# Optimization experiments

Measured on AMD Instinct MI355X. Metric: run time of the kernel, lower is better.

The kernel has to match this reference:

```python
import jax, jax.numpy as jnp
import numpy as np

B, D, C, N = 256, 512, 345, 50000
K = 5
ALPHA = 1.0
EPS = 1e-12


def setup_inputs() -> dict:
    key = jax.random.key(0)
    k1, k2, k3, k4, k5 = jax.random.split(key, 5)
    return {
        "features": jax.random.normal(k1, (B, D), dtype=jnp.float32),
        "predictions": jax.random.normal(k2, (B, C), dtype=jnp.float32),
        "fea_bank": jax.random.normal(k3, (N, D), dtype=jnp.float32),
        "score_bank": jax.random.uniform(k4, (N, C), dtype=jnp.float32, minval=1e-3, maxval=1.0),
        "trg_idx": jax.random.randint(k5, (B,), 0, N, dtype=jnp.int64),
    }


def reference(features, predictions, fea_bank, score_bank, trg_idx):
    softmax_out = jax.nn.softmax(predictions, axis=1)  # [B, C]

    # --- no_grad block: bank update + neighbor retrieval ---
    f_norm = features / jnp.maximum(
        jnp.linalg.norm(features, axis=1, keepdims=True), EPS
    )
    f_ng = jax.lax.stop_gradient(f_norm)
    s_ng = jax.lax.stop_gradient(softmax_out)
    fb = fea_bank.at[trg_idx].set(f_ng)       # [N, D]
    sb = score_bank.at[trg_idx].set(s_ng)     # [N, C]
    distance = f_ng @ fb.T                    # [B, N] cosine similarity
    _, idx_near = jax.lax.top_k(distance, K + 1)
    idx_near = idx_near[:, 1:]                # drop self -> [B, K]
    score_near = sb[idx_near]                 # [B, K, C]

    # F.kl_div(input=softmax_out (NOT log), target=score_near):
    # target * (log(target) - input), summed over C and K, mean over B.
    kl = score_near * (jnp.log(score_near) - softmax_out[:, None, :])
    loss = jnp.mean(kl.sum(-1).sum(-1))

    # dispersion: masked pairwise dot of softmax outputs (off-diagonal)
    dot = softmax_out @ softmax_out.T         # [B, B]
    mask = 1.0 - jnp.eye(B, dtype=dot.dtype)
    neg_pred = jnp.mean((dot * mask).sum(-1))
    loss = loss + ALPHA * neg_pred
    return loss
```

## Files before the change

kernel.cpp:

```cpp
#include <hip/hip_runtime.h>
#include <cstdint>

#define BB 256
#define DD 512
#define CC 345
#define NBANK 50000
#define NPAD 50048
#define KNEI 5
#define ALPHAC 1.0f
#define EPSN 1e-12f
#define NTILES 391

typedef short short8 __attribute__((ext_vector_type(8)));
typedef float f32x4 __attribute__((ext_vector_type(4)));

__device__ inline uint32_t f2bf1(float x) {
    union { float f; uint32_t u; } v; v.f = x;
    return (v.u + 0x7FFFu + ((v.u >> 16) & 1u)) >> 16;
}
__device__ inline uint32_t pack2(float a, float b) {
    return f2bf1(a) | (f2bf1(b) << 16);
}
__device__ inline float bl(uint32_t x) {
    union { uint32_t u; float f; } v; v.u = x << 16; return v.f;
}
__device__ inline float bh(uint32_t x) {
    union { uint32_t u; float f; } v; v.u = x & 0xFFFF0000u; return v.f;
}
__device__ inline bool better(float v1, int i1, float v2, int i2) {
    return (v1 > v2) || (v1 == v2 && i1 < i2);
}
__device__ inline void ins6(float v, int j, float* lv, int* li) {
    if (better(v, j, lv[5], li[5])) {
        int q = 5;
        while (q > 0 && better(v, j, lv[q - 1], li[q - 1])) {
            lv[q] = lv[q - 1]; li[q] = li[q - 1]; q--;
        }
        lv[q] = v; li[q] = j;
    }
}
__device__ inline void tree6(float* sv, int* si, int t, const float* lv, const int* li) {
#pragma unroll
    for (int r = 0; r < 6; r++) { sv[t * 6 + r] = lv[r]; si[t * 6 + r] = li[r]; }
    __syncthreads();
    for (int s = 128; s > 0; s >>= 1) {
        if (t < s) {
            float av[6], bv[6], rv[6];
            int ai[6], bi[6], ri[6];
#pragma unroll
            for (int r = 0; r < 6; r++) {
                av[r] = sv[t * 6 + r];       ai[r] = si[t * 6 + r];
                bv[r] = sv[(t + s) * 6 + r]; bi[r] = si[(t + s) * 6 + r];
            }
            int x = 0, y = 0;
#pragma unroll
            for (int o = 0; o < 6; o++) {
                if (better(av[x], ai[x], bv[y], bi[y])) { rv[o] = av[x]; ri[o] = ai[x]; x++; }
                else                                    { rv[o] = bv[y]; ri[o] = bi[y]; y++; }
            }
#pragma unroll
            for (int r = 0; r < 6; r++) { sv[t * 6 + r] = rv[r]; si[t * 6 + r] = ri[r]; }
        }
        __syncthreads();
    }
}
__device__ inline void async16(const void* g, void* l) {
    __builtin_amdgcn_global_load_lds(
        (const __attribute__((address_space(1))) unsigned int*)g,
        (__attribute__((address_space(3))) unsigned int*)l, 16, 0, 0);
}
__device__ inline size_t sw_off(int tile, int r, int ch) {
    return (size_t)tile * 8192 + r * 64 + ((ch ^ (r & 7)) * 8);
}

__global__ void winner_kernel(const int* __restrict__ trg, int* __restrict__ win,
                              float* __restrict__ out) {
    int t = threadIdx.x;
    if (t == 0) out[0] = 0.f;
    int mv = trg[t];
    int w = 1;
    for (int b2 = t + 1; b2 < BB; b2++)
        if (trg[b2] == mv) w = 0;
    win[t] = w;
}

__global__ void norm_softmax_kernel(const float* __restrict__ feat,
                                    const float* __restrict__ pred,
                                    unsigned short* __restrict__ fnb,
                                    unsigned short* __restrict__ fnb2,
                                    float* __restrict__ p) {
    int b = blockIdx.x, t = threadIdx.x;
    __shared__ float red[256];
    float x0 = feat[b * DD + t];
    float x1 = feat[b * DD + t + 256];
    red[t] = x0 * x0 + x1 * x1;
    __syncthreads();
    for (int s = 128; s > 0; s >>= 1) {
        if (t < s) red[t] += red[t + s];
        __syncthreads();
    }
    float inv = 1.0f / fmaxf(sqrtf(red[0]), EPSN);
    if (t < 64) {
        const f32x4* src = (const f32x4*)(feat + b * DD + t * 8);
        f32x4 f0 = src[0], f1 = src[1];
        uint4 u = make_uint4(pack2(f0[0] * inv, f0[1] * inv),
                             pack2(f0[2] * inv, f0[3] * inv),
                             pack2(f1[0] * inv, f1[1] * inv),
                             pack2(f1[2] * inv, f1[3] * inv));
        *(uint4*)(fnb + b * DD + t * 8) = u;
        int mtile = b >> 7, r = b & 127, kt = t >> 3, ch = t & 7;
        *(uint4*)(fnb2 + sw_off(mtile * 8 + kt, r, ch)) = u;
    }
    __syncthreads();
    float y0 = (t < CC) ? pred[b * CC + t] : -3.0e38f;
    float y1 = (t + 256 < CC) ? pred[b * CC + t + 256] : -3.0e38f;
    red[t] = fmaxf(y0, y1);
    __syncthreads();
    for (int s = 128; s > 0; s >>= 1) {
        if (t < s) red[t] = fmaxf(red[t], red[t + s]);
        __syncthreads();
    }
    float M = red[0];
    __syncthreads();
    float e0 = (t < CC) ? expf(y0 - M) : 0.f;
    float e1 = (t + 256 < CC) ? expf(y1 - M) : 0.f;
    red[t] = e0 + e1;
    __syncthreads();
    for (int s = 128; s > 0; s >>= 1) {
        if (t < s) red[t] += red[t + s];
        __syncthreads();
    }
    float si = 1.0f / red[0];
    if (t < CC) p[b * CC + t] = e0 * si;
    if (t + 256 < CC) p[b * CC + t + 256] = e1 * si;
}

__global__ void convert_kernel(const float* __restrict__ bank,
                               unsigned short* __restrict__ bankb) {
    int tid = blockIdx.x * 256 + threadIdx.x;
    int j = tid >> 6, c = tid & 63;
    int kt = c >> 3, ch = c & 7;
    int r = j & 127, nt = j >> 7;
    uint4 val = make_uint4(0, 0, 0, 0);
    if (j < NBANK) {
        const f32x4* s = (const f32x4*)(bank + (size_t)j * DD + kt * 64 + ch * 8);
        f32x4 f0 = s[0], f1 = s[1];
        val = make_uint4(pack2(f0[0], f0[1]), pack2(f0[2], f0[3]),
                         pack2(f1[0], f1[1]), pack2(f1[2], f1[3]));
    }
    *(uint4*)(bankb + sw_off(nt * 8 + kt, r, ch)) = val;
}

__global__ void patch_kernel(const unsigned short* __restrict__ fnb,
                             const int* __restrict__ trg, const int* __restrict__ win,
                             unsigned short* __restrict__ bankb) {
    int b = blockIdx.x;
    if (!win[b]) return;
    int t = threadIdx.x;
    int j = trg[b];
    int nt = j >> 7, r = j & 127, kt = t >> 3, ch = t & 7;
    uint4 v = *(const uint4*)(fnb + b * DD + t * 8);
    *(uint4*)(bankb + sw_off(nt * 8 + kt, r, ch)) = v;
}

__global__ __launch_bounds__(256) void gemm_topk_kernel(
        const unsigned short* __restrict__ fnb2, const unsigned short* __restrict__ bankb,
        float* __restrict__ tilemax) {
    __shared__ __align__(16) char smem[32768];
    unsigned short* As = (unsigned short*)smem;
    unsigned short* Bs = (unsigned short*)(smem + 16384);

    int t = threadIdx.x;
    int ntb = blockIdx.x >> 1, mtile = blockIdx.x & 1;
    int w = t >> 6, lane = t & 63, quad = lane >> 4, l16 = lane & 15;
    int wm = w >> 1, wn = w & 1;
    int j0 = ntb * 128;

    f32x4 acc[4][4];
#pragma unroll
    for (int mt = 0; mt < 4; mt++)
#pragma unroll
        for (int nt = 0; nt < 4; nt++)
            acc[mt][nt] = (f32x4){0.f, 0.f, 0.f, 0.f};

    const char* Ag = (const char*)fnb2 + (size_t)mtile * 8 * 16384;
    const char* Bg = (const char*)bankb + (size_t)ntb * 8 * 16384;

    for (int kt = 0; kt < 8; kt++) {
        size_t tb = (size_t)kt * 16384;
        int co = w * 4096 + lane * 16;
#pragma unroll
        for (int u = 0; u < 4; u++)
            async16(Ag + tb + co + u * 1024, smem + w * 4096 + u * 1024);
#pragma unroll
        for (int u = 0; u < 4; u++)
            async16(Bg + tb + co + u * 1024, smem + 16384 + w * 4096 + u * 1024);
        __syncthreads();
#pragma unroll
        for (int ks = 0; ks < 2; ks++) {
            int sw = ((ks * 4 + quad) ^ (l16 & 7)) * 8;
            short8 af[4], bf[4];
#pragma unroll
            for (int mt = 0; mt < 4; mt++)
                af[mt] = *(const short8*)(As + (wm * 64 + mt * 16 + l16) * 64 + sw);
#pragma unroll
            for (int nt = 0; nt < 4; nt++)
                bf[nt] = *(const short8*)(Bs + (wn * 64 + nt * 16 + l16) * 64 + sw);
#pragma unroll
            for (int mt = 0; mt < 4; mt++)
#pragma unroll
                for (int nt = 0; nt < 4; nt++)
                    acc[mt][nt] = __builtin_amdgcn_mfma_f32_16x16x32_bf16(
                        af[mt], bf[nt], acc[mt][nt], 0, 0, 0);
        }
        __syncthreads();
    }

    bool maskPad[4] = {false, false, false, false};
    if (ntb == NTILES - 1) {
#pragma unroll
        for (int nt = 0; nt < 4; nt++)
            maskPad[nt] = (j0 + wn * 64 + nt * 16 + l16) >= NBANK;
    }
    float* sm = (float*)smem;
#pragma unroll
    for (int mt = 0; mt < 4; mt++)
#pragma unroll
        for (int r2 = 0; r2 < 4; r2++) {
            float m = -3.4e38f;
#pragma unroll
            for (int nt = 0; nt < 4; nt++) {
                float v = maskPad[nt] ? -3.4e38f : acc[mt][nt][r2];
                m = fmaxf(m, v);
            }
#pragma unroll
            for (int off = 1; off < 16; off <<= 1)
                m = fmaxf(m, __shfl_xor(m, off, 64));
            if (l16 == 0) sm[(wm * 64 + mt * 16 + quad * 4 + r2) * 2 + wn] = m;
        }
    __syncthreads();
    if (t < 128)
        tilemax[(size_t)ntb * 256 + mtile * 128 + t] = fmaxf(sm[t * 2], sm[t * 2 + 1]);
}

__global__ void merge_rescan_kernel(const unsigned short* __restrict__ fnb,
                                    const unsigned short* __restrict__ bankb,
                                    const float* __restrict__ tilemax,
                                    int* __restrict__ nidx) {
    int i = blockIdx.x, t = threadIdx.x;
    __shared__ float a[512];
    __shared__ float tm[512];
    __shared__ int cand[NTILES + 1];
    __shared__ int ncand;
    __shared__ float sv[1536];
    __shared__ int si[1536];

    uint32_t wrd = ((const uint32_t*)(fnb + (size_t)i * DD))[t];
    a[2 * t] = bl(wrd);
    a[2 * t + 1] = bh(wrd);
    tm[t] = (t < NTILES) ? tilemax[(size_t)t * 256 + i] : -3.4e38f;
    tm[t + 256] = (t + 256 < NTILES) ? tilemax[(size_t)(t + 256) * 256 + i] : -3.4e38f;
    if (t == 0) ncand = 0;
    __syncthreads();

    float lv[6]; int li[6];
#pragma unroll
    for (int r = 0; r < 6; r++) { lv[r] = -3.4e38f; li[r] = 0x7FFFFFFF; }
    ins6(tm[t], t, lv, li);
    ins6(tm[t + 256], t + 256, lv, li);
    tree6(sv, si, t, lv, li);
    float M6 = sv[5];
    __syncthreads();

    if (t < NTILES && tm[t] >= M6) cand[atomicAdd(&ncand, 1)] = t;
    if (t + 256 < NTILES && tm[t + 256] >= M6) cand[atomicAdd(&ncand, 1)] = t + 256;
    __syncthreads();
    int nc = ncand;

#pragma unroll
    for (int r = 0; r < 6; r++) { lv[r] = -3.4e38f; li[r] = 0x7FFFFFFF; }
    int r = t & 127;
    int rx = r & 7;
    for (int c0 = 0; c0 < nc; c0 += 2) {
        int slot = c0 + (t >> 7);
        if (slot < nc) {
            int nt = cand[slot];
            int j = nt * 128 + r;
            if (j < NBANK) {
                float dot = 0.f;
#pragma unroll
                for (int kt = 0; kt < 8; kt++) {
                    const uint4* q = (const uint4*)(bankb + (size_t)(nt * 8 + kt) * 8192 + r * 64);
                    const float* ab = a + kt * 64;
#pragma unroll
                    for (int pp = 0; pp < 8; pp++) {
                        uint4 u = q[pp];
                        const float* av = ab + ((pp ^ rx) << 3);
                        dot += bl(u.x) * av[0] + bh(u.x) * av[1]
                             + bl(u.y) * av[2] + bh(u.y) * av[3]
                             + bl(u.z) * av[4] + bh(u.z) * av[5]
                             + bl(u.w) * av[6] + bh(u.w) * av[7];
                    }
                }
                ins6(dot, j, lv, li);
            }
        }
    }
    tree6(sv, si, t, lv, li);
    if (t == 0) {
#pragma unroll
        for (int rr = 1; rr < 6; rr++) nidx[i * KNEI + rr - 1] = si[rr];
    }
}

__global__ void kl_negpred_kernel(const float* __restrict__ p,
                                  const float* __restrict__ sbank,
                                  const int* __restrict__ nidx,
                                  const int* __restrict__ trg,
                                  float* __restrict__ out) {
    int bid = blockIdx.x, t = threadIdx.x;
    __shared__ float red[256];
    __shared__ float aux[256];
    if (bid < BB) {
        int b = bid;
        __shared__ int sj[KNEI], sb[KNEI];
        if (t < KNEI) {
            int j = nidx[b * KNEI + t];
            sj[t] = j;
            int src = -1;
            for (int b2 = 0; b2 < BB; b2++)
                if (trg[b2] == j) src = b2;
            sb[t] = src;
        }
        __syncthreads();
        float local = 0.f;
        for (int k = 0; k < KNEI; k++) {
            int j = sj[k], src = sb[k];
            const float* srow = (src >= 0) ? (p + src * CC) : (sbank + (size_t)j * CC);
            for (int c = t; c < CC; c += 256) {
                float s = srow[c];
                local += s * (logf(s) - p[b * CC + c]);
            }
        }
        red[t] = local;
        __syncthreads();
        for (int s = 128; s > 0; s >>= 1) {
            if (t < s) red[t] += red[t + s];
            __syncthreads();
        }
        if (t == 0) atomicAdd(out, red[0] * (1.0f / BB));
    } else {
        int c = bid - BB;
        float v = p[t * CC + c];
        red[t] = v;
        aux[t] = v * v;
        __syncthreads();
        for (int s = 128; s > 0; s >>= 1) {
            if (t < s) { red[t] += red[t + s]; aux[t] += aux[t + s]; }
            __syncthreads();
        }
        if (t == 0) atomicAdd(out, ALPHAC * (red[0] * red[0] - aux[0]) * (1.0f / BB));
    }
}

extern "C" void kernel_launch(void* const* d_in, const int* in_sizes, int n_in,
                              void* d_out, int out_size, void* d_ws, size_t ws_size,
                              hipStream_t stream) {
    const float* feat  = (const float*)d_in[0];
    const float* pred  = (const float*)d_in[1];
    const float* bank  = (const float*)d_in[2];
    const float* sbank = (const float*)d_in[3];
    const int*   trg   = (const int*)d_in[4];
    float* out = (float*)d_out;

    char* ws = (char*)d_ws;
    unsigned short* fnb2    = (unsigned short*)ws;
    unsigned short* fnb     = (unsigned short*)(ws + 262144);
    unsigned short* bankb   = (unsigned short*)(ws + 524288);
    float*          p       = (float*)(ws + 51773440);
    int*            win     = (int*)(ws + 52126720);
    float*          tilemax = (float*)(ws + 52127744);
    int*            nidx    = (int*)(ws + 52528128);

    winner_kernel<<<1, 256, 0, stream>>>(trg, win, out);
    norm_softmax_kernel<<<BB, 256, 0, stream>>>(feat, pred, fnb, fnb2, p);
    convert_kernel<<<(NPAD * 64) / 256, 256, 0, stream>>>(bank, bankb);
    patch_kernel<<<BB, 64, 0, stream>>>(fnb, trg, win, bankb);
    gemm_topk_kernel<<<NTILES * 2, 256, 0, stream>>>(fnb2, bankb, tilemax);
    merge_rescan_kernel<<<BB, 256, 0, stream>>>(fnb, bankb, tilemax, nidx);
    kl_negpred_kernel<<<BB + CC, 256, 0, stream>>>(p, sbank, nidx, trg, out);
}
```

Baseline: 292.0 us.

## Emit per-half-tile top-2 keys from GEMM to shrink rescan in merge

The GEMM epilogue now records, for each row and each 64-column half tile, the top two packed (value, index) 64-bit keys instead of a single tile max. The merge kernel selects the top 6 among these keys and rescans only the half tiles whose second-best key reaches the sixth-best threshold, which should usually be none. The goal is to remove most of the exact dot-product rescan over whole 128-column candidate tiles. It also stages trg in shared memory in two small kernels. In exchange it writes a larger candidate buffer and caps the rescan list at 128 half tiles.

After: 284.3 us. 2.6% less time.

```diff
diff --git a/kernel.cpp b/kernel.cpp
--- a/kernel.cpp
+++ b/kernel.cpp
@@ -10,9 +10,12 @@
 #define ALPHAC 1.0f
 #define EPSN 1e-12f
 #define NTILES 391
+#define NHALF (NTILES * 2)
+#define CSLOTS (NTILES * 4)
 
 typedef short short8 __attribute__((ext_vector_type(8)));
 typedef float f32x4 __attribute__((ext_vector_type(4)));
+typedef unsigned long long u64;
 
 __device__ inline uint32_t f2bf1(float x) {
     union { float f; uint32_t u; } v; v.f = x;
@@ -27,39 +30,43 @@
 __device__ inline float bh(uint32_t x) {
     union { uint32_t u; float f; } v; v.u = x & 0xFFFF0000u; return v.f;
 }
-__device__ inline bool better(float v1, int i1, float v2, int i2) {
-    return (v1 > v2) || (v1 == v2 && i1 < i2);
-}
-__device__ inline void ins6(float v, int j, float* lv, int* li) {
-    if (better(v, j, lv[5], li[5])) {
+__device__ inline u64 mkkey(float v, int j) {
+    union { float f; uint32_t u; } c; c.f = v;
+    uint32_t b = c.u;
+    uint32_t k = (b & 0x80000000u) ? ~b : (b | 0x80000000u);
+    return ((u64)k << 32) | (uint32_t)(~j);
+}
+__device__ inline u64 umax64(u64 a, u64 b) { return a > b ? a : b; }
+__device__ inline u64 shfl_xor_u64(u64 v, int m) {
+    int lo = __shfl_xor((int)(uint32_t)v, m, 64);
+    int hi = __shfl_xor((int)(v >> 32), m, 64);
+    return ((u64)(uint32_t)hi << 32) | (uint32_t)lo;
+}
+__device__ inline void ins6u(u64 k, u64* lv) {
+    if (k > lv[5]) {
         int q = 5;
-        while (q > 0 && better(v, j, lv[q - 1], li[q - 1])) {
-            lv[q] = lv[q - 1]; li[q] = li[q - 1]; q--;
-        }
-        lv[q] = v; li[q] = j;
-    }
-}
-__device__ inline void tree6(float* sv, int* si, int t, const float* lv, const int* li) {
-#pragma unroll
-    for (int r = 0; r < 6; r++) { sv[t * 6 + r] = lv[r]; si[t * 6 + r] = li[r]; }
+        while (q > 0 && k > lv[q - 1]) { lv[q] = lv[q - 1]; q--; }
+        lv[q] = k;
+    }
+}
+__device__ inline void tree6u(u64* sv, int t, const u64* lv) {
+#pragma unroll
+    for (int r = 0; r < 6; r++) sv[t * 6 + r] = lv[r];
     __syncthreads();
     for (int s = 128; s > 0; s >>= 1) {
         if (t < s) {
-            float av[6], bv[6], rv[6];
-            int ai[6], bi[6], ri[6];
-#pragma unroll
-            for (int r = 0; r < 6; r++) {
-                av[r] = sv[t * 6 + r];       ai[r] = si[t * 6 + r];
-                bv[r] = sv[(t + s) * 6 + r]; bi[r] = si[(t + s) * 6 + r];
+            u64 av[6], bv[6], rv[6];
+#pragma unroll
+            for (int r = 0; r < 6; r++) { av[r] = sv[t * 6 + r]; bv[r] = sv[(t + s) * 6 + r]; }
+            int x = 0, y = 0;
+#pragma unroll
+            for (int o = 0; o < 6; o++) {
+                bool pk = av[x] > bv[y];
+                rv[o] = pk ? av[x] : bv[y];
+                x += pk; y += !pk;
             }
-            int x = 0, y = 0;
-#pragma unroll
-            for (int o = 0; o < 6; o++) {
-                if (better(av[x], ai[x], bv[y], bi[y])) { rv[o] = av[x]; ri[o] = ai[x]; x++; }
-                else                                    { rv[o] = bv[y]; ri[o] = bi[y]; y++; }
-            }
-#pragma unroll
-            for (int r = 0; r < 6; r++) { sv[t * 6 + r] = rv[r]; si[t * 6 + r] = ri[r]; }
+#pragma unroll
+            for (int r = 0; r < 6; r++) sv[t * 6 + r] = rv[r];
         }
         __syncthreads();
     }
@@ -76,11 +83,14 @@
 __global__ void winner_kernel(const int* __restrict__ trg, int* __restrict__ win,
                               float* __restrict__ out) {
     int t = threadIdx.x;
+    __shared__ int st[BB];
     if (t == 0) out[0] = 0.f;
-    int mv = trg[t];
+    st[t] = trg[t];
+    __syncthreads();
+    int mv = st[t];
     int w = 1;
     for (int b2 = t + 1; b2 < BB; b2++)
-        if (trg[b2] == mv) w = 0;
+        if (st[b2] == mv) w = 0;
     win[t] = w;
 }
 
@@ -165,7 +175,7 @@
 
 __global__ __launch_bounds__(256) void gemm_topk_kernel(
         const unsigned short* __restrict__ fnb2, const unsigned short* __restrict__ bankb,
-        float* __restrict__ tilemax) {
+        u64* __restrict__ cand) {
     __shared__ __align__(16) char smem[32768];
     unsigned short* As = (unsigned short*)smem;
     unsigned short* Bs = (unsigned short*)(smem + 16384);
@@ -216,100 +226,110 @@
         __syncthreads();
     }
 
-    bool maskPad[4] = {false, false, false, false};
-    if (ntb == NTILES - 1) {
-#pragma unroll
-        for (int nt = 0; nt < 4; nt++)
-            maskPad[nt] = (j0 + wn * 64 + nt * 16 + l16) >= NBANK;
-    }
-    float* sm = (float*)smem;
+    bool maskPad[4];
+#pragma unroll
+    for (int nt = 0; nt < 4; nt++)
+        maskPad[nt] = (ntb == NTILES - 1) && ((j0 + wn * 64 + nt * 16 + l16) >= NBANK);
+
 #pragma unroll
     for (int mt = 0; mt < 4; mt++)
 #pragma unroll
         for (int r2 = 0; r2 < 4; r2++) {
-            float m = -3.4e38f;
+            u64 k[4];
 #pragma unroll
             for (int nt = 0; nt < 4; nt++) {
-                float v = maskPad[nt] ? -3.4e38f : acc[mt][nt][r2];
-                m = fmaxf(m, v);
+                int j = j0 + wn * 64 + nt * 16 + l16;
+                k[nt] = maskPad[nt] ? 0ull : mkkey(acc[mt][nt][r2], j);
             }
+            u64 m = umax64(umax64(k[0], k[1]), umax64(k[2], k[3]));
 #pragma unroll
             for (int off = 1; off < 16; off <<= 1)
-                m = fmaxf(m, __shfl_xor(m, off, 64));
-            if (l16 == 0) sm[(wm * 64 + mt * 16 + quad * 4 + r2) * 2 + wn] = m;
-        }
-    __syncthreads();
-    if (t < 128)
-        tilemax[(size_t)ntb * 256 + mtile * 128 + t] = fmaxf(sm[t * 2], sm[t * 2 + 1]);
-}
-
-__global__ void merge_rescan_kernel(const unsigned short* __restrict__ fnb,
-                                    const unsigned short* __restrict__ bankb,
-                                    const float* __restrict__ tilemax,
-                                    int* __restrict__ nidx) {
+                m = umax64(m, shfl_xor_u64(m, off));
+            u64 top1 = m;
+#pragma unroll
+            for (int nt = 0; nt < 4; nt++) k[nt] = (k[nt] == top1) ? 0ull : k[nt];
+            m = umax64(umax64(k[0], k[1]), umax64(k[2], k[3]));
+#pragma unroll
+            for (int off = 1; off < 16; off <<= 1)
+                m = umax64(m, shfl_xor_u64(m, off));
+            if (l16 == 0) {
+                int gi = mtile * 128 + wm * 64 + mt * 16 + quad * 4 + r2;
+                u64* cp = cand + (size_t)gi * CSLOTS + (ntb * 2 + wn) * 2;
+                cp[0] = top1; cp[1] = m;
+            }
+        }
+}
+
+__global__ __launch_bounds__(256) void merge_kernel(
+        const u64* __restrict__ cand, const unsigned short* __restrict__ fnb,
+        const unsigned short* __restrict__ bankb, int* __restrict__ nidx) {
     int i = blockIdx.x, t = threadIdx.x;
+    __shared__ u64 sv[1536];
+    __shared__ uint32_t fm[25];
+    __shared__ int fl[128];
+    __shared__ int nf;
     __shared__ float a[512];
-    __shared__ float tm[512];
-    __shared__ int cand[NTILES + 1];
-    __shared__ int ncand;
-    __shared__ float sv[1536];
-    __shared__ int si[1536];
-
-    uint32_t wrd = ((const uint32_t*)(fnb + (size_t)i * DD))[t];
-    a[2 * t] = bl(wrd);
-    a[2 * t + 1] = bh(wrd);
-    tm[t] = (t < NTILES) ? tilemax[(size_t)t * 256 + i] : -3.4e38f;
-    tm[t + 256] = (t + 256 < NTILES) ? tilemax[(size_t)(t + 256) * 256 + i] : -3.4e38f;
-    if (t == 0) ncand = 0;
-    __syncthreads();
-
-    float lv[6]; int li[6];
-#pragma unroll
-    for (int r = 0; r < 6; r++) { lv[r] = -3.4e38f; li[r] = 0x7FFFFFFF; }
-    ins6(tm[t], t, lv, li);
-    ins6(tm[t + 256], t + 256, lv, li);
-    tree6(sv, si, t, lv, li);
-    float M6 = sv[5];
-    __syncthreads();
-
-    if (t < NTILES && tm[t] >= M6) cand[atomicAdd(&ncand, 1)] = t;
-    if (t + 256 < NTILES && tm[t + 256] >= M6) cand[atomicAdd(&ncand, 1)] = t + 256;
-    __syncthreads();
-    int nc = ncand;
-
-#pragma unroll
-    for (int r = 0; r < 6; r++) { lv[r] = -3.4e38f; li[r] = 0x7FFFFFFF; }
-    int r = t & 127;
-    int rx = r & 7;
-    for (int c0 = 0; c0 < nc; c0 += 2) {
-        int slot = c0 + (t >> 7);
-        if (slot < nc) {
-            int nt = cand[slot];
-            int j = nt * 128 + r;
-            if (j < NBANK) {
-                float dot = 0.f;
-#pragma unroll
-                for (int kt = 0; kt < 8; kt++) {
-                    const uint4* q = (const uint4*)(bankb + (size_t)(nt * 8 + kt) * 8192 + r * 64);
-                    const float* ab = a + kt * 64;
-#pragma unroll
-                    for (int pp = 0; pp < 8; pp++) {
-                        uint4 u = q[pp];
-                        const float* av = ab + ((pp ^ rx) << 3);
-                        dot += bl(u.x) * av[0] + bh(u.x) * av[1]
-                             + bl(u.y) * av[2] + bh(u.y) * av[3]
-                             + bl(u.z) * av[4] + bh(u.z) * av[5]
-                             + bl(u.w) * av[6] + bh(u.w) * av[7];
+    const u64* cr = cand + (size_t)i * CSLOTS;
+
+    u64 lv[6] = {0, 0, 0, 0, 0, 0};
+    for (int q = t; q < CSLOTS; q += 256) ins6u(cr[q], lv);
+    if (t < 25) fm[t] = 0;
+    if (t == 0) nf = 0;
+    tree6u(sv, t, lv);
+    u64 M6 = sv[5];
+    __syncthreads();
+    for (int h = t; h < NHALF; h += 256) {
+        if (cr[h * 2 + 1] >= M6) {
+            int s = atomicAdd(&nf, 1);
+            if (s < 128) fl[s] = h;
+            atomicOr(&fm[h >> 5], 1u << (h & 31));
+        }
+    }
+    __syncthreads();
+    if (nf > 0) {
+        uint32_t wrd = ((const uint32_t*)(fnb + (size_t)i * DD))[t];
+        a[2 * t] = bl(wrd);
+        a[2 * t + 1] = bh(wrd);
+        __syncthreads();
+        u64 l2[6] = {0, 0, 0, 0, 0, 0};
+        for (int q = t; q < CSLOTS; q += 256) {
+            int h = q >> 1;
+            if (!((fm[h >> 5] >> (h & 31)) & 1u)) ins6u(cr[q], l2);
+        }
+        int nfl = nf < 128 ? nf : 128;
+        for (int s = 0; s < nfl; s++) {
+            int h = fl[s];
+            if (t < 64) {
+                int nt2 = h >> 1;
+                int r = (h & 1) * 64 + t;
+                int j = nt2 * 128 + r;
+                if (j < NBANK) {
+                    int rx = r & 7;
+                    float dot = 0.f;
+                    for (int kt = 0; kt < 8; kt++) {
+                        const uint4* q4 = (const uint4*)(bankb + (size_t)(nt2 * 8 + kt) * 8192 + r * 64);
+                        const float* ab = a + kt * 64;
+#pragma unroll
+                        for (int pp = 0; pp < 8; pp++) {
+                            uint4 u = q4[pp];
+                            const float* av = ab + ((pp ^ rx) << 3);
+                            dot += bl(u.x) * av[0] + bh(u.x) * av[1]
+                                 + bl(u.y) * av[2] + bh(u.y) * av[3]
+                                 + bl(u.z) * av[4] + bh(u.z) * av[5]
+                                 + bl(u.w) * av[6] + bh(u.w) * av[7];
+                        }
                     }
+                    ins6u(mkkey(dot, j), l2);
                 }
-                ins6(dot, j, lv, li);
             }
         }
-    }
-    tree6(sv, si, t, lv, li);
+        __syncthreads();
+        tree6u(sv, t, l2);
+    }
     if (t == 0) {
 #pragma unroll
-        for (int rr = 1; rr < 6; rr++) nidx[i * KNEI + rr - 1] = si[rr];
+        for (int r = 1; r < 6; r++)
+            nidx[i * KNEI + r - 1] = (int)(~(uint32_t)(sv[r] & 0xFFFFFFFFull));
     }
 }
 
@@ -323,13 +343,16 @@
     __shared__ float aux[256];
     if (bid < BB) {
         int b = bid;
+        __shared__ int st[BB];
         __shared__ int sj[KNEI], sb[KNEI];
+        st[t] = trg[t];
+        __syncthreads();
         if (t < KNEI) {
             int j = nidx[b * KNEI + t];
             sj[t] = j;
             int src = -1;
             for (int b2 = 0; b2 < BB; b2++)
-                if (trg[b2] == j) src = b2;
+                if (st[b2] == j) src = b2;
             sb[t] = src;
         }
         __syncthreads();
@@ -374,19 +397,19 @@
     float* out = (float*)d_out;
 
     char* ws = (char*)d_ws;
-    unsigned short* fnb2    = (unsigned short*)ws;
-    unsigned short* fnb     = (unsigned short*)(ws + 262144);
-    unsigned short* bankb   = (unsigned short*)(ws + 524288);
-    float*          p       = (float*)(ws + 51773440);
-    int*            win     = (int*)(ws + 52126720);
-    float*          tilemax = (float*)(ws + 52127744);
-    int*            nidx    = (int*)(ws + 52528128);
+    unsigned short* fnb2  = (unsigned short*)ws;
+    unsigned short* fnb   = (unsigned short*)(ws + 262144);
+    unsigned short* bankb = (unsigned short*)(ws + 524288);
+    float*          p     = (float*)(ws + 51773440);
+    int*            win   = (int*)(ws + 52126720);
+    u64*            cand  = (u64*)(ws + 52127744);
+    int*            nidx  = (int*)(ws + 55330816);
 
     winner_kernel<<<1, 256, 0, stream>>>(trg, win, out);
     norm_softmax_kernel<<<BB, 256, 0, stream>>>(feat, pred, fnb, fnb2, p);
     convert_kernel<<<(NPAD * 64) / 256, 256, 0, stream>>>(bank, bankb);
     patch_kernel<<<BB, 64, 0, stream>>>(fnb, trg, win, bankb);
-    gemm_topk_kernel<<<NTILES * 2, 256, 0, stream>>>(fnb2, bankb, tilemax);
-    merge_rescan_kernel<<<BB, 256, 0, stream>>>(fnb, bankb, tilemax, nidx);
+    gemm_topk_kernel<<<NTILES * 2, 256, 0, stream>>>(fnb2, bankb, cand);
+    merge_kernel<<<BB, 256, 0, stream>>>(cand, fnb, bankb, nidx);
     kl_negpred_kernel<<<BB + CC, 256, 0, stream>>>(p, sbank, nidx, trg, out);
 }
```
